# Kernel tuning notes

Measured on AMD Instinct MI355X. Metric: run time of the kernel, lower is better.

Reference implementation:

```python
import jax, jax.numpy as jnp
import numpy as np

N, E, G = 150000, 600000, 5000
NI, EI, GF, H, C = 16, 8, 32, 64, 40


def setup_inputs() -> dict:
    key = jax.random.key(0)
    ks = jax.random.split(key, 20)
    s = lambda fan: 1.0 / np.sqrt(fan)
    return {
        "x": jax.random.normal(ks[0], (N, NI), jnp.float32),
        "edge_index": jax.random.randint(ks[1], (2, E), 0, N),
        "edge_attr": jax.random.normal(ks[2], (E, EI), jnp.float32),
        "batch": jnp.sort(jax.random.randint(ks[3], (N,), 0, G)),
        "pocket_features": jax.random.normal(ks[4], (G, GF), jnp.float32),
        # edge MLP: Linear(EI,H) -> ReLU -> Linear(H, H*NI)
        "W_e1": jax.random.normal(ks[5], (EI, H), jnp.float32) * s(EI),
        "b_e1": jnp.zeros((H,), jnp.float32),
        "W_e2": jax.random.normal(ks[6], (H, H * NI), jnp.float32) * s(H),
        "b_e2": jnp.zeros((H * NI,), jnp.float32),
        # NNConv root weight + bias
        "root": jax.random.normal(ks[7], (NI, H), jnp.float32) * s(NI),
        "conv_bias": jnp.zeros((H,), jnp.float32),
        # GlobalAttention gate Linear(H,1)
        "Wg": jax.random.normal(ks[8], (H, 1), jnp.float32) * s(H),
        "bg": jnp.zeros((1,), jnp.float32),
        # fc1: input is concat [h_node(H), global_ctx(H), pocket(GF)]
        "W_fc1": jax.random.normal(ks[9], (2 * H + GF, H), jnp.float32) * s(2 * H + GF),
        "b_fc1": jnp.zeros((H,), jnp.float32),
        "W_np": jax.random.normal(ks[10], (H, C), jnp.float32) * s(H),
        "b_np": jnp.zeros((C,), jnp.float32),
        "W_sp": jax.random.normal(ks[11], (H, 1), jnp.float32) * s(H),
        "b_sp": jnp.zeros((1,), jnp.float32),
    }


def reference(x, edge_index, edge_attr, batch, pocket_features,
              W_e1, b_e1, W_e2, b_e2, root, conv_bias, Wg, bg,
              W_fc1, b_fc1, W_np, b_np, W_sp, b_sp):
    n, ni = x.shape
    h = root.shape[1]
    g = pocket_features.shape[0]
    src, dst = edge_index[0], edge_index[1]

    # NNConv: edge MLP -> per-edge weight matrix [E, NI, H]
    eh = jax.nn.relu(edge_attr @ W_e1 + b_e1)
    We = (eh @ W_e2 + b_e2).reshape(-1, ni, h)
    msg = jnp.einsum('ei,eih->eh', x[src], We)          # per-edge matmul
    agg = jax.ops.segment_sum(msg, dst, num_segments=n)
    cnt = jax.ops.segment_sum(jnp.ones(msg.shape[0], x.dtype), dst, num_segments=n)
    agg = agg / jnp.maximum(cnt, 1.0)[:, None]          # aggr='mean'
    h_node = jax.nn.relu(agg + x @ root + conv_bias)    # [N, H]

    # GlobalAttention pooling: scatter-softmax over nodes per graph
    gate = (h_node @ Wg + bg).squeeze(-1)               # [N]
    m = jax.ops.segment_max(gate, batch, num_segments=g)
    e = jnp.exp(gate - m[batch])
    denom = jax.ops.segment_sum(e, batch, num_segments=g)
    attn = e / denom[batch]
    gctx = jax.ops.segment_sum(attn[:, None] * h_node, batch, num_segments=g)
    gc = gctx[batch]                                    # broadcast back [N, H]

    feat = jnp.concatenate([h_node, gc, pocket_features[batch]], axis=1)
    f = jax.nn.relu(feat @ W_fc1 + b_fc1)
    node_pred = jax.nn.log_softmax(f @ W_np + b_np, axis=-1)
    stop = jax.nn.sigmoid((gc @ W_sp + b_sp).squeeze(-1))
    return node_pred, stop
```

## Files before the change

kernel.cpp:

```cpp
#include <hip/hip_runtime.h>
#include <hip/hip_bf16.h>
#include <math.h>

#define NN 150000
#define EE 600000
#define GG 5000
#define NI 16
#define EI 8
#define GFD 32
#define HH 64
#define CC 40

#define W2SZ (68 * 1024)
#define FPAD 68
#define NBLK ((NN + 1023) / 1024)

typedef __attribute__((ext_vector_type(8))) short short8v;
typedef __attribute__((ext_vector_type(16))) float f32x16;
typedef __attribute__((ext_vector_type(2))) float f32x2;

__device__ __forceinline__ unsigned short f2bf(float f) {
    __hip_bfloat16 h = __float2bfloat16(f);
    return __builtin_bit_cast(unsigned short, h);
}
__device__ __forceinline__ float bf2f(unsigned short u) {
    return __uint_as_float(((unsigned)u) << 16);
}
__device__ __forceinline__ unsigned cvtpk(float lo, float hi) {
    unsigned r;
    asm("v_cvt_pk_bf16_f32 %0, %1, %2" : "=v"(r) : "v"(lo), "v"(hi));
    return r;
}
__device__ __forceinline__ f32x2 pkmul(f32x2 a, f32x2 b) {
    f32x2 p;
    asm("v_pk_mul_f32 %0, %1, %2" : "=v"(p) : "v"(a), "v"(b));
    return p;
}
__device__ __forceinline__ short8v zfrag(float eh, const f32x2 (&xs2)[4]) {
    f32x2 ehp; ehp[0] = eh; ehp[1] = eh;
    union { short8v v; unsigned u[4]; } A;
    #pragma unroll
    for (int q = 0; q < 4; ++q) {
        f32x2 p = pkmul(ehp, xs2[q]);
        A.u[q] = cvtpk(p[0], p[1]);
    }
    return A.v;
}
__device__ __forceinline__ short8v xfrag(const f32x2 (&xs2)[4]) {
    union { short8v v; unsigned u[4]; } A;
    #pragma unroll
    for (int q = 0; q < 4; ++q)
        A.u[q] = cvtpk(xs2[q][0], xs2[q][1]);
    return A.v;
}

__global__ void k0_prep(const float* __restrict__ W_e2, const float* __restrict__ b_e2,
                        const float* __restrict__ W_fc1, const float* __restrict__ W_np,
                        unsigned short* __restrict__ W2c,
                        unsigned short* __restrict__ W1aT,
                        unsigned short* __restrict__ W_npT,
                        int* __restrict__ cursor)
{
    int idx = blockIdx.x * 256 + threadIdx.x;
    if (idx < W2SZ) {
        int c = idx >> 10, rem = idx & 1023;
        int r = rem >> 4, kk = rem & 15;
        float v = 0.f;
        if (c < 64)       v = W_e2[c * 1024 + kk * 64 + r];
        else if (c == 64) v = b_e2[kk * 64 + r];
        W2c[idx] = f2bf(v);
    } else if (idx < W2SZ + 4096) {
        int i = idx - W2SZ;
        int h = i >> 6, k = i & 63;
        W1aT[i] = f2bf(W_fc1[k * 64 + h]);
    } else if (idx < W2SZ + 8192) {
        int i = idx - W2SZ - 4096;
        int c = i >> 6, h = i & 63;
        W_npT[i] = f2bf(c < CC ? W_np[h * CC + c] : 0.f);
    } else if (idx < W2SZ + 8192 + NN) {
        cursor[idx - W2SZ - 8192] = 0;
    }
}

__global__ void kE_local(const int* __restrict__ ei, int* __restrict__ cursor,
                         int* __restrict__ rank)
{
    int e = blockIdx.x * 256 + threadIdx.x;
    if (e < EE) rank[e] = atomicAdd(&cursor[ei[EE + e]], 1);
}

__global__ void kB_scan1(const int* __restrict__ cnt, int* __restrict__ base,
                         int* __restrict__ bsum)
{
    __shared__ int sS[256];
    int b = blockIdx.x, t = threadIdx.x;
    int i0 = b * 1024 + t * 4;
    int v0 = (i0 + 0 < NN) ? cnt[i0 + 0] : 0;
    int v1 = (i0 + 1 < NN) ? cnt[i0 + 1] : 0;
    int v2 = (i0 + 2 < NN) ? cnt[i0 + 2] : 0;
    int v3 = (i0 + 3 < NN) ? cnt[i0 + 3] : 0;
    int tot = v0 + v1 + v2 + v3;
    sS[t] = tot;
    __syncthreads();
    int acc = tot;
    for (int off = 1; off < 256; off <<= 1) {
        int xv = (t >= off) ? sS[t - off] : 0;
        __syncthreads();
        acc += xv;
        sS[t] = acc;
        __syncthreads();
    }
    int run = acc - tot;
    if (i0 + 0 < NN) base[i0 + 0] = run; run += v0;
    if (i0 + 1 < NN) base[i0 + 1] = run; run += v1;
    if (i0 + 2 < NN) base[i0 + 2] = run; run += v2;
    if (i0 + 3 < NN) base[i0 + 3] = run;
    if (t == 255) bsum[b] = acc;
}

__global__ void kC_scan2(int* __restrict__ bsum)
{
    __shared__ int sS[256];
    int t = threadIdx.x;
    int v = (t < NBLK) ? bsum[t] : 0;
    sS[t] = v;
    __syncthreads();
    int acc = v;
    for (int off = 1; off < 256; off <<= 1) {
        int xv = (t >= off) ? sS[t - off] : 0;
        __syncthreads();
        acc += xv;
        sS[t] = acc;
        __syncthreads();
    }
    if (t < NBLK) bsum[t] = acc - v;
}

__global__ void kD_scan3(int* __restrict__ base, const int* __restrict__ bsum)
{
    int i = blockIdx.x * 256 + threadIdx.x;
    if (i < NN) base[i] = base[i] + bsum[i >> 10];
    if (i == 0) base[NN] = EE;
}

__device__ __forceinline__ void mfma_step(
    const unsigned short (&sEHT)[65][256], int c, int pf,
    const unsigned short* __restrict__ Bq0, const unsigned short* __restrict__ Bq1,
    int mb, int mr, const f32x2 (&xs0)[4], const f32x2 (&xs1)[4],
    short8v& curb0, short8v& curb1,
    f32x16& acc00, f32x16& acc01, f32x16& acc10, f32x16& acc11)
{
    short8v n0 = *(const short8v*)(Bq0 + pf * 1024);
    short8v n1 = *(const short8v*)(Bq1 + pf * 1024);
    int cc = (c & 31) << 1;
    float eh0 = bf2f(sEHT[c][(mb + mr) ^ cc]);
    float eh1 = bf2f(sEHT[c][(mb + 32 + mr) ^ cc]);
    short8v a0 = zfrag(eh0, xs0);
    short8v a1 = zfrag(eh1, xs1);
    __builtin_amdgcn_s_setprio(1);
    acc00 = __builtin_amdgcn_mfma_f32_32x32x16_bf16(a0, curb0, acc00, 0, 0, 0);
    acc01 = __builtin_amdgcn_mfma_f32_32x32x16_bf16(a0, curb1, acc01, 0, 0, 0);
    acc10 = __builtin_amdgcn_mfma_f32_32x32x16_bf16(a1, curb0, acc10, 0, 0, 0);
    acc11 = __builtin_amdgcn_mfma_f32_32x32x16_bf16(a1, curb1, acc11, 0, 0, 0);
    __builtin_amdgcn_s_setprio(0);
    curb0 = n0; curb1 = n1;
}

template<bool TWOPHASE>
__global__ __launch_bounds__(256, 4) void k1_mfma(
    const float* __restrict__ x, const int* __restrict__ ei,
    const float* __restrict__ ea,
    const float* __restrict__ W_e1, const float* __restrict__ b_e1,
    const unsigned short* __restrict__ W2c,
    const int* __restrict__ rank, const int* __restrict__ base,
    unsigned* __restrict__ msg16, float* __restrict__ agg)
{
    __shared__ unsigned short sEHT[65][256];
    __shared__ int sIdx[256];

    const int t = threadIdx.x;
    const long long eb = (long long)blockIdx.x * 256;

    {
        long long ge = eb + t;
        if (ge < EE) {
            int d = ei[EE + ge];
            sIdx[t] = TWOPHASE ? (base[d] + rank[ge]) : d;
        } else {
            sIdx[t] = -1;
        }
        sEHT[64][t] = (unsigned short)0x3F80;
    }
    {
        const int k = t & 63;
        const int w = t >> 6;
        float w1[8];
        float b1 = b_e1[k];
        #pragma unroll
        for (int j = 0; j < 8; ++j) w1[j] = W_e1[j * 64 + k];
        #pragma unroll 4
        for (int r = 0; r < 64; ++r) {
            int e = w * 64 + r;
            long long ge = eb + e;
            float v = 0.f;
            if (ge < EE) {
                const float4* eap = (const float4*)(ea + ge * EI);
                float4 u0 = eap[0], u1 = eap[1];
                v = b1;
                v = fmaf(u0.x, w1[0], v); v = fmaf(u0.y, w1[1], v);
                v = fmaf(u0.z, w1[2], v); v = fmaf(u0.w, w1[3], v);
                v = fmaf(u1.x, w1[4], v); v = fmaf(u1.y, w1[5], v);
                v = fmaf(u1.z, w1[6], v); v = fmaf(u1.w, w1[7], v);
                v = fmaxf(v, 0.f);
            }
            sEHT[k][e ^ ((k & 31) << 1)] = f2bf(v);
        }
    }

    const int lane = t & 63;
    const int w = t >> 6;
    const int mr = lane & 31;
    const int half = lane >> 5;
    const int mb = w * 64;

    f32x2 xs0[4], xs1[4];
    {
        long long e0 = eb + mb + mr;
        long long e1 = eb + mb + 32 + mr;
        if (e0 < EE) {
            int s0 = ei[e0];
            const float4* xp = (const float4*)(x + (size_t)s0 * NI + half * 8);
            float4 u0 = xp[0], u1 = xp[1];
            xs0[0][0]=u0.x; xs0[0][1]=u0.y; xs0[1][0]=u0.z; xs0[1][1]=u0.w;
            xs0[2][0]=u1.x; xs0[2][1]=u1.y; xs0[3][0]=u1.z; xs0[3][1]=u1.w;
        } else {
            #pragma unroll
            for (int q = 0; q < 4; ++q) { xs0[q][0] = 0.f; xs0[q][1] = 0.f; }
        }
        if (e1 < EE) {
            int s1 = ei[e1];
            const float4* xp = (const float4*)(x + (size_t)s1 * NI + half * 8);
            float4 u0 = xp[0], u1 = xp[1];
            xs1[0][0]=u0.x; xs1[0][1]=u0.y; xs1[1][0]=u0.z; xs1[1][1]=u0.w;
            xs1[2][0]=u1.x; xs1[2][1]=u1.y; xs1[3][0]=u1.z; xs1[3][1]=u1.w;
        } else {
            #pragma unroll
            for (int q = 0; q < 4; ++q) { xs1[q][0] = 0.f; xs1[q][1] = 0.f; }
        }
    }
    __syncthreads();

    f32x16 acc00, acc01, acc10, acc11;
    #pragma unroll
    for (int r = 0; r < 16; ++r) { acc00[r] = 0.f; acc01[r] = 0.f; acc10[r] = 0.f; acc11[r] = 0.f; }

    const unsigned short* Bq0 = W2c + mr * 16 + half * 8;
    const unsigned short* Bq1 = Bq0 + 512;

    short8v bA0 = *(const short8v*)(Bq0);
    short8v bA1 = *(const short8v*)(Bq1);
    short8v bB0 = *(const short8v*)(Bq0 + 1024);
    short8v bB1 = *(const short8v*)(Bq1 + 1024);

    #pragma unroll 2
    for (int c = 0; c < 64; c += 2) {
        mfma_step(sEHT, c,     c + 2, Bq0, Bq1, mb, mr, xs0, xs1, bA0, bA1, acc00, acc01, acc10, acc11);
        mfma_step(sEHT, c + 1, c + 3, Bq0, Bq1, mb, mr, xs0, xs1, bB0, bB1, acc00, acc01, acc10, acc11);
    }
    {
        short8v a0 = xfrag(xs0);
        short8v a1 = xfrag(xs1);
        __builtin_amdgcn_s_setprio(1);
        acc00 = __builtin_amdgcn_mfma_f32_32x32x16_bf16(a0, bA0, acc00, 0, 0, 0);
        acc01 = __builtin_amdgcn_mfma_f32_32x32x16_bf16(a0, bA1, acc01, 0, 0, 0);
        acc10 = __builtin_amdgcn_mfma_f32_32x32x16_bf16(a1, bA0, acc10, 0, 0, 0);
        acc11 = __builtin_amdgcn_mfma_f32_32x32x16_bf16(a1, bA1, acc11, 0, 0, 0);
        __builtin_amdgcn_s_setprio(0);
    }

    #pragma unroll
    for (int r = 0; r < 16; ++r) {
        int row = (r & 3) + 8 * (r >> 2) + 4 * half;
        int i0 = sIdx[mb + row];
        int i1 = sIdx[mb + 32 + row];
        if (TWOPHASE) {
            if (i0 >= 0) msg16[(size_t)i0 * 32 + mr] = cvtpk(acc00[r], acc01[r]);
            if (i1 >= 0) msg16[(size_t)i1 * 32 + mr] = cvtpk(acc10[r], acc11[r]);
        } else {
            if (i0 >= 0) {
                atomicAdd(&agg[(size_t)i0 * 64 + mr],      acc00[r]);
                atomicAdd(&agg[(size_t)i0 * 64 + 32 + mr], acc01[r]);
            }
            if (i1 >= 0) {
                atomicAdd(&agg[(size_t)i1 * 64 + mr],      acc10[r]);
                atomicAdd(&agg[(size_t)i1 * 64 + 32 + mr], acc11[r]);
            }
        }
    }
}

__global__ __launch_bounds__(256) void k2_red(
    const unsigned* __restrict__ msg16, const int* __restrict__ base,
    const float* __restrict__ x, const float* __restrict__ root,
    const float* __restrict__ conv_bias,
    unsigned short* __restrict__ hn16,
    const float* __restrict__ Wg, const float* __restrict__ bg,
    float* __restrict__ gate)
{
    __shared__ float sroot[16][64];
    int t = threadIdx.x;
    #pragma unroll
    for (int q = 0; q < 4; ++q) {
        int i = q * 256 + t;
        sroot[i >> 6][i & 63] = root[i];
    }
    __syncthreads();

    int n = blockIdx.x * 4 + (t >> 6);
    int l = t & 63;
    int mr = l & 31, so = l >> 5;
    int s = base[n], e = base[n + 1];

    float alo = 0.f, ahi = 0.f;
    for (int sl = s + so; sl < e; sl += 2) {
        unsigned u = msg16[(size_t)sl * 32 + mr];
        alo += __uint_as_float(u << 16);
        ahi += __uint_as_float(u & 0xFFFF0000u);
    }
    alo += __shfl_xor(alo, 32);
    ahi += __shfl_xor(ahi, 32);
    float acc = (l < 32) ? alo : ahi;

    float inv = 1.0f / fmaxf((float)(e - s), 1.0f);
    float v = acc * inv + conv_bias[l];
    float xv = (l < 16) ? x[(size_t)n * NI + l] : 0.f;
    #pragma unroll
    for (int i = 0; i < 16; ++i)
        v = fmaf(__shfl(xv, i), sroot[i][l], v);
    v = fmaxf(v, 0.f);
    hn16[(size_t)n * 64 + l] = f2bf(v);

    float gv = v * Wg[l];
    #pragma unroll
    for (int off = 32; off; off >>= 1) gv += __shfl_xor(gv, off);
    if (l == 0) gate[n] = gv + bg[0];
}

__global__ __launch_bounds__(256) void k2_node(
    const float* __restrict__ agg, const int* __restrict__ base,
    const float* __restrict__ x, const float* __restrict__ root,
    const float* __restrict__ conv_bias,
    unsigned short* __restrict__ hn16,
    const float* __restrict__ Wg, const float* __restrict__ bg,
    float* __restrict__ gate)
{
    int t = threadIdx.x;
    int n = blockIdx.x * 4 + (t >> 6);
    int h = t & 63;
    float cntv = (float)(base[n + 1] - base[n]);
    float inv = 1.0f / fmaxf(cntv, 1.0f);
    float v = agg[(size_t)n * 64 + h] * inv + conv_bias[h];
    const float* xp = x + (size_t)n * NI;
    #pragma unroll
    for (int i = 0; i < NI; ++i) v += xp[i] * root[i * 64 + h];
    v = fmaxf(v, 0.f);
    hn16[(size_t)n * 64 + h] = f2bf(v);
    float gv = v * Wg[h];
    #pragma unroll
    for (int off = 32; off; off >>= 1) gv += __shfl_xor(gv, off);
    if (h == 0) gate[n] = gv + bg[0];
}

__device__ __forceinline__ int lbound(const int* __restrict__ b, int v) {
    int lo = 0, hi = NN;
    while (lo < hi) { int mid = (lo + hi) >> 1; if (b[mid] < v) lo = mid + 1; else hi = mid; }
    return lo;
}

__global__ __launch_bounds__(64) void k3_pool(
    const float* __restrict__ gate, const int* __restrict__ batch,
    const unsigned short* __restrict__ hn16, const float* __restrict__ pocket,
    const float* __restrict__ W_fc1, const float* __restrict__ b_fc1,
    const float* __restrict__ W_sp, const float* __restrict__ b_sp,
    float* __restrict__ pg, float* __restrict__ sg)
{
    int g = blockIdx.x;
    int lane = threadIdx.x;
    int s = lbound(batch, g);
    int e = lbound(batch, g + 1);

    float gcv = 0.f;
    if (e > s) {
        float m = -INFINITY;
        for (int n = s + lane; n < e; n += 64) m = fmaxf(m, gate[n]);
        #pragma unroll
        for (int off = 32; off; off >>= 1) m = fmaxf(m, __shfl_xor(m, off));
        float acc = 0.f, den = 0.f;
        for (int n = s; n < e; ++n) {
            float ev = expf(gate[n] - m);
            den += ev;
            acc += ev * bf2f(hn16[(size_t)n * 64 + lane]);
        }
        gcv = acc / den;
    }

    float sv = gcv * W_sp[lane];
    #pragma unroll
    for (int off = 32; off; off >>= 1) sv += __shfl_xor(sv, off);
    if (lane == 0) sg[g] = 1.f / (1.f + expf(-(sv + b_sp[0])));

    float pk = (lane < GFD) ? pocket[(size_t)g * GFD + lane] : 0.f;
    float pgv = b_fc1[lane];
    #pragma unroll 8
    for (int kk = 0; kk < 64; ++kk)
        pgv = fmaf(__shfl(gcv, kk), W_fc1[(64 + kk) * 64 + lane], pgv);
    #pragma unroll 8
    for (int kk = 0; kk < 32; ++kk)
        pgv = fmaf(__shfl(pk, kk), W_fc1[(128 + kk) * 64 + lane], pgv);
    pg[(size_t)g * 64 + lane] = pgv;
}

__global__ __launch_bounds__(256, 4) void k4_mfma(
    const unsigned short* __restrict__ hn16, const int* __restrict__ batch,
    const float* __restrict__ pg, const float* __restrict__ sg,
    const unsigned short* __restrict__ W1aT, const unsigned short* __restrict__ W_npT,
    const float* __restrict__ b_np,
    float* __restrict__ out_np, float* __restrict__ out_stop)
{
    __shared__ __align__(16) float sF[4][32][FPAD];
    __shared__ int sB[128];

    const int t = threadIdx.x;
    const int wv = t >> 6, lane = t & 63;
    const int mr = lane & 31, half = lane >> 5;
    const int nb = blockIdx.x * 128;

    if (t < 128) {
        int n = nb + t;
        sB[t] = (n < NN) ? batch[n] : 0;
    }

    const int node = nb + wv * 32 + mr;

    f32x16 acc0, acc1;
    #pragma unroll
    for (int r = 0; r < 16; ++r) { acc0[r] = 0.f; acc1[r] = 0.f; }

    #pragma unroll
    for (int c = 0; c < 4; ++c) {
        short8v a;
        if (node < NN) {
            a = *(const short8v*)(hn16 + (size_t)node * 64 + c * 16 + half * 8);
        } else {
            #pragma unroll
            for (int q = 0; q < 8; ++q) a[q] = 0;
        }
        short8v b0 = *(const short8v*)(W1aT + (size_t)mr * 64        + c * 16 + half * 8);
        short8v b1 = *(const short8v*)(W1aT + (size_t)(mr + 32) * 64 + c * 16 + half * 8);
        acc0 = __builtin_amdgcn_mfma_f32_32x32x16_bf16(a, b0, acc0, 0, 0, 0);
        acc1 = __builtin_amdgcn_mfma_f32_32x32x16_bf16(a, b1, acc1, 0, 0, 0);
    }
    __syncthreads();

    #pragma unroll
    for (int r = 0; r < 16; ++r) {
        int row = (r & 3) + 8 * (r >> 2) + 4 * half;
        int g = sB[wv * 32 + row];
        float p0 = pg[(size_t)g * 64 + mr];
        float p1 = pg[(size_t)g * 64 + 32 + mr];
        sF[wv][row][mr]      = fmaxf(acc0[r] + p0, 0.f);
        sF[wv][row][32 + mr] = fmaxf(acc1[r] + p1, 0.f);
    }

    f32x16 acc2, acc3;
    #pragma unroll
    for (int r = 0; r < 16; ++r) { acc2[r] = 0.f; acc3[r] = 0.f; }

    #pragma unroll
    for (int c = 0; c < 4; ++c) {
        const float* fp = &sF[wv][mr][c * 16 + half * 8];
        float4 u0 = *(const float4*)(fp);
        float4 u1 = *(const float4*)(fp + 4);
        union { short8v v; unsigned u[4]; } A;
        A.u[0] = cvtpk(u0.x, u0.y); A.u[1] = cvtpk(u0.z, u0.w);
        A.u[2] = cvtpk(u1.x, u1.y); A.u[3] = cvtpk(u1.z, u1.w);
        short8v a = A.v;
        short8v b0 = *(const short8v*)(W_npT + (size_t)mr * 64        + c * 16 + half * 8);
        short8v b1 = *(const short8v*)(W_npT + (size_t)(mr + 32) * 64 + c * 16 + half * 8);
        acc2 = __builtin_amdgcn_mfma_f32_32x32x16_bf16(a, b0, acc2, 0, 0, 0);
        acc3 = __builtin_amdgcn_mfma_f32_32x32x16_bf16(a, b1, acc3, 0, 0, 0);
    }

    float bn1 = b_np[mr];
    float bn2 = (mr < 8) ? b_np[32 + mr] : 0.f;

    #pragma unroll
    for (int r = 0; r < 16; ++r) {
        int row = (r & 3) + 8 * (r >> 2) + 4 * half;
        int n = nb + wv * 32 + row;
        float v1 = acc2[r] + bn1;
        float v2 = acc3[r] + bn2;
        float m = (mr < 8) ? fmaxf(v1, v2) : v1;
        #pragma unroll
        for (int off = 16; off; off >>= 1) m = fmaxf(m, __shfl_xor(m, off));
        float s = expf(v1 - m) + ((mr < 8) ? expf(v2 - m) : 0.f);
        #pragma unroll
        for (int off = 16; off; off >>= 1) s += __shfl_xor(s, off);
        float ls = m + logf(s);
        if (n < NN) {
            out_np[(size_t)n * CC + mr] = v1 - ls;
            if (mr < 8) out_np[(size_t)n * CC + 32 + mr] = v2 - ls;
            if (mr == 0) out_stop[n] = sg[sB[wv * 32 + row]];
        }
    }
}

extern "C" void kernel_launch(void* const* d_in, const int* in_sizes, int n_in,
                              void* d_out, int out_size, void* d_ws, size_t ws_size,
                              hipStream_t stream)
{
    (void)in_sizes; (void)n_in; (void)out_size;
    const float* x        = (const float*)d_in[0];
    const int*   ei       = (const int*)d_in[1];
    const float* ea       = (const float*)d_in[2];
    const int*   batch    = (const int*)d_in[3];
    const float* pocket   = (const float*)d_in[4];
    const float* W_e1     = (const float*)d_in[5];
    const float* b_e1     = (const float*)d_in[6];
    const float* W_e2     = (const float*)d_in[7];
    const float* b_e2     = (const float*)d_in[8];
    const float* root     = (const float*)d_in[9];
    const float* conv_b   = (const float*)d_in[10];
    const float* Wg       = (const float*)d_in[11];
    const float* bg       = (const float*)d_in[12];
    const float* W_fc1    = (const float*)d_in[13];
    const float* b_fc1    = (const float*)d_in[14];
    const float* W_np     = (const float*)d_in[15];
    const float* b_np     = (const float*)d_in[16];
    const float* W_sp     = (const float*)d_in[17];
    const float* b_sp     = (const float*)d_in[18];

    char* wsb = (char*)d_ws;
    float* agg    = (float*)wsb;
    int*   base   = (int*)(agg + (size_t)NN * 64);
    int*   bsum   = base + NN + 4;
    int*   cursor = bsum + 256;
    int*   rank   = cursor + NN;
    float* gate   = (float*)(rank + EE);
    float* pg     = gate + NN;
    float* sg     = pg + (size_t)GG * 64;
    unsigned short* hn16  = (unsigned short*)(sg + GG);
    unsigned short* W2c   = hn16 + (size_t)NN * 64;
    unsigned short* W1aT  = W2c + W2SZ;
    unsigned short* W_npT = W1aT + 4096;
    size_t head = (size_t)((char*)(W_npT + 4096) - wsb);
    size_t msg_off = (head + 255) & ~(size_t)255;
    unsigned* msg16 = (unsigned*)(wsb + msg_off);
    size_t need = msg_off + (size_t)EE * 32 * sizeof(unsigned);
    const bool twophase = (ws_size >= need);

    k0_prep<<<(W2SZ + 8192 + NN + 255) / 256, 256, 0, stream>>>(
        W_e2, b_e2, W_fc1, W_np, W2c, W1aT, W_npT, cursor);

    kE_local<<<(EE + 255) / 256, 256, 0, stream>>>(ei, cursor, rank);
    kB_scan1<<<NBLK, 256, 0, stream>>>(cursor, base, bsum);
    kC_scan2<<<1, 256, 0, stream>>>(bsum);
    kD_scan3<<<(NN + 255) / 256, 256, 0, stream>>>(base, bsum);

    if (twophase) {
        k1_mfma<true><<<(EE + 255) / 256, 256, 0, stream>>>(
            x, ei, ea, W_e1, b_e1, W2c, rank, base, msg16, agg);
        k2_red<<<NN / 4, 256, 0, stream>>>(msg16, base, x, root, conv_b,
                                           hn16, Wg, bg, gate);
    } else {
        hipMemsetAsync(agg, 0, (size_t)NN * 64 * sizeof(float), stream);
        k1_mfma<false><<<(EE + 255) / 256, 256, 0, stream>>>(
            x, ei, ea, W_e1, b_e1, W2c, rank, base, msg16, agg);
        k2_node<<<NN / 4, 256, 0, stream>>>(agg, base, x, root, conv_b, hn16, Wg, bg, gate);
    }

    k3_pool<<<GG, 64, 0, stream>>>(gate, batch, hn16, pocket, W_fc1, b_fc1, W_sp, b_sp, pg, sg);

    float* out_np   = (float*)d_out;
    float* out_stop = out_np + (size_t)NN * CC;
    k4_mfma<<<(NN + 127) / 128, 256, 0, stream>>>(hn16, batch, pg, sg, W1aT, W_npT, b_np,
                                                  out_np, out_stop);
}
```

Before: 297.5 us.

## Compute edge MLP first layer with MFMA and fold scan fixup into consumers

```diff
diff --git a/kernel.cpp b/kernel.cpp
--- a/kernel.cpp
+++ b/kernel.cpp
@@ -56,9 +56,11 @@
 
 __global__ void k0_prep(const float* __restrict__ W_e2, const float* __restrict__ b_e2,
                         const float* __restrict__ W_fc1, const float* __restrict__ W_np,
+                        const float* __restrict__ W_e1,
                         unsigned short* __restrict__ W2c,
                         unsigned short* __restrict__ W1aT,
                         unsigned short* __restrict__ W_npT,
+                        unsigned short* __restrict__ W1e,
                         int* __restrict__ cursor)
 {
     int idx = blockIdx.x * 256 + threadIdx.x;
@@ -77,8 +79,12 @@
         int i = idx - W2SZ - 4096;
         int c = i >> 6, h = i & 63;
         W_npT[i] = f2bf(c < CC ? W_np[h * CC + c] : 0.f);
-    } else if (idx < W2SZ + 8192 + NN) {
-        cursor[idx - W2SZ - 8192] = 0;
+    } else if (idx < W2SZ + 8704) {
+        int i = idx - W2SZ - 8192;
+        int col = i >> 3, q = i & 7;
+        W1e[i] = f2bf(W_e1[q * 64 + col]);
+    } else if (idx < W2SZ + 8704 + NN) {
+        cursor[idx - W2SZ - 8704] = 0;
     }
 }
 
@@ -136,13 +142,6 @@
     if (t < NBLK) bsum[t] = acc - v;
 }
 
-__global__ void kD_scan3(int* __restrict__ base, const int* __restrict__ bsum)
-{
-    int i = blockIdx.x * 256 + threadIdx.x;
-    if (i < NN) base[i] = base[i] + bsum[i >> 10];
-    if (i == 0) base[NN] = EE;
-}
-
 __device__ __forceinline__ void mfma_step(
     const unsigned short (&sEHT)[65][256], int c, int pf,
     const unsigned short* __restrict__ Bq0, const unsigned short* __restrict__ Bq1,
@@ -170,9 +169,10 @@
 __global__ __launch_bounds__(256, 4) void k1_mfma(
     const float* __restrict__ x, const int* __restrict__ ei,
     const float* __restrict__ ea,
-    const float* __restrict__ W_e1, const float* __restrict__ b_e1,
+    const unsigned short* __restrict__ W1e, const float* __restrict__ b_e1,
     const unsigned short* __restrict__ W2c,
     const int* __restrict__ rank, const int* __restrict__ base,
+    const int* __restrict__ bsum,
     unsigned* __restrict__ msg16, float* __restrict__ agg)
 {
     __shared__ unsigned short sEHT[65][256];
@@ -180,48 +180,70 @@
 
     const int t = threadIdx.x;
     const long long eb = (long long)blockIdx.x * 256;
-
-    {
-        long long ge = eb + t;
-        if (ge < EE) {
-            int d = ei[EE + ge];
-            sIdx[t] = TWOPHASE ? (base[d] + rank[ge]) : d;
-        } else {
-            sIdx[t] = -1;
-        }
-        sEHT[64][t] = (unsigned short)0x3F80;
-    }
-    {
-        const int k = t & 63;
-        const int w = t >> 6;
-        float w1[8];
-        float b1 = b_e1[k];
-        #pragma unroll
-        for (int j = 0; j < 8; ++j) w1[j] = W_e1[j * 64 + k];
-        #pragma unroll 4
-        for (int r = 0; r < 64; ++r) {
-            int e = w * 64 + r;
-            long long ge = eb + e;
-            float v = 0.f;
-            if (ge < EE) {
-                const float4* eap = (const float4*)(ea + ge * EI);
-                float4 u0 = eap[0], u1 = eap[1];
-                v = b1;
-                v = fmaf(u0.x, w1[0], v); v = fmaf(u0.y, w1[1], v);
-                v = fmaf(u0.z, w1[2], v); v = fmaf(u0.w, w1[3], v);
-                v = fmaf(u1.x, w1[4], v); v = fmaf(u1.y, w1[5], v);
-                v = fmaf(u1.z, w1[6], v); v = fmaf(u1.w, w1[7], v);
-                v = fmaxf(v, 0.f);
-            }
-            sEHT[k][e ^ ((k & 31) << 1)] = f2bf(v);
-        }
-    }
 
     const int lane = t & 63;
     const int w = t >> 6;
     const int mr = lane & 31;
     const int half = lane >> 5;
     const int mb = w * 64;
+
+    {
+        long long ge = eb + t;
+        if (ge < EE) {
+            int d = ei[EE + ge];
+            sIdx[t] = TWOPHASE ? (base[d] + bsum[d >> 10] + rank[ge]) : d;
+        } else {
+            sIdx[t] = -1;
+        }
+        sEHT[64][t] = (unsigned short)0x3F80;
+    }
+
+    {
+        short8v bW0, bW1;
+        if (half == 0) {
+            bW0 = *(const short8v*)(W1e + (size_t)mr * 8);
+            bW1 = *(const short8v*)(W1e + (size_t)(32 + mr) * 8);
+        } else {
+            #pragma unroll
+            for (int q = 0; q < 8; ++q) { bW0[q] = 0; bW1[q] = 0; }
+        }
+        float bias0 = b_e1[mr];
+        float bias1 = b_e1[32 + mr];
+        #pragma unroll
+        for (int m = 0; m < 2; ++m) {
+            int e_loc = w * 64 + m * 32 + mr;
+            long long ge = eb + e_loc;
+            short8v a;
+            if (half == 0 && ge < EE) {
+                const float4* eap = (const float4*)(ea + ge * EI);
+                float4 u0 = eap[0], u1 = eap[1];
+                union { short8v v; unsigned u[4]; } A;
+                A.u[0] = cvtpk(u0.x, u0.y); A.u[1] = cvtpk(u0.z, u0.w);
+                A.u[2] = cvtpk(u1.x, u1.y); A.u[3] = cvtpk(u1.z, u1.w);
+                a = A.v;
+            } else {
+                #pragma unroll
+                for (int q = 0; q < 8; ++q) a[q] = 0;
+            }
+            #pragma unroll
+            for (int n = 0; n < 2; ++n) {
+                f32x16 c_;
+                #pragma unroll
+                for (int r = 0; r < 16; ++r) c_[r] = 0.f;
+                c_ = __builtin_amdgcn_mfma_f32_32x32x16_bf16(a, n ? bW1 : bW0, c_, 0, 0, 0);
+                int kcol = n * 32 + mr;
+                float bias = n ? bias1 : bias0;
+                #pragma unroll
+                for (int r = 0; r < 16; r += 2) {
+                    int row = (r & 3) + 8 * (r >> 2) + 4 * half;
+                    int e0 = w * 64 + m * 32 + row;
+                    float v0 = fmaxf(c_[r]     + bias, 0.f);
+                    float v1 = fmaxf(c_[r + 1] + bias, 0.f);
+                    *(unsigned*)&sEHT[kcol][e0 ^ (mr << 1)] = cvtpk(v0, v1);
+                }
+            }
+        }
+    }
 
     f32x2 xs0[4], xs1[4];
     {
@@ -301,6 +323,7 @@
 
 __global__ __launch_bounds__(256) void k2_red(
     const unsigned* __restrict__ msg16, const int* __restrict__ base,
+    const int* __restrict__ bsum,
     const float* __restrict__ x, const float* __restrict__ root,
     const float* __restrict__ conv_bias,
     unsigned short* __restrict__ hn16,
@@ -319,7 +342,8 @@
     int n = blockIdx.x * 4 + (t >> 6);
     int l = t & 63;
     int mr = l & 31, so = l >> 5;
-    int s = base[n], e = base[n + 1];
+    int s = base[n] + bsum[n >> 10];
+    int e = (n == NN - 1) ? EE : base[n + 1] + bsum[(n + 1) >> 10];
 
     float alo = 0.f, ahi = 0.f;
     for (int sl = s + so; sl < e; sl += 2) {
@@ -348,6 +372,7 @@
 
 __global__ __launch_bounds__(256) void k2_node(
     const float* __restrict__ agg, const int* __restrict__ base,
+    const int* __restrict__ bsum,
     const float* __restrict__ x, const float* __restrict__ root,
     const float* __restrict__ conv_bias,
     unsigned short* __restrict__ hn16,
@@ -357,8 +382,9 @@
     int t = threadIdx.x;
     int n = blockIdx.x * 4 + (t >> 6);
     int h = t & 63;
-    float cntv = (float)(base[n + 1] - base[n]);
-    float inv = 1.0f / fmaxf(cntv, 1.0f);
+    int s = base[n] + bsum[n >> 10];
+    int e = (n == NN - 1) ? EE : base[n + 1] + bsum[(n + 1) >> 10];
+    float inv = 1.0f / fmaxf((float)(e - s), 1.0f);
     float v = agg[(size_t)n * 64 + h] * inv + conv_bias[h];
     const float* xp = x + (size_t)n * NI;
     #pragma unroll
@@ -553,30 +579,31 @@
     unsigned short* W2c   = hn16 + (size_t)NN * 64;
     unsigned short* W1aT  = W2c + W2SZ;
     unsigned short* W_npT = W1aT + 4096;
-    size_t head = (size_t)((char*)(W_npT + 4096) - wsb);
+    unsigned short* W1e   = W_npT + 4096;
+    size_t head = (size_t)((char*)(W1e + 512) - wsb);
     size_t msg_off = (head + 255) & ~(size_t)255;
     unsigned* msg16 = (unsigned*)(wsb + msg_off);
     size_t need = msg_off + (size_t)EE * 32 * sizeof(unsigned);
     const bool twophase = (ws_size >= need);
 
-    k0_prep<<<(W2SZ + 8192 + NN + 255) / 256, 256, 0, stream>>>(
-        W_e2, b_e2, W_fc1, W_np, W2c, W1aT, W_npT, cursor);
+    k0_prep<<<(W2SZ + 8704 + NN + 255) / 256, 256, 0, stream>>>(
+        W_e2, b_e2, W_fc1, W_np, W_e1, W2c, W1aT, W_npT, W1e, cursor);
 
     kE_local<<<(EE + 255) / 256, 256, 0, stream>>>(ei, cursor, rank);
     kB_scan1<<<NBLK, 256, 0, stream>>>(cursor, base, bsum);
     kC_scan2<<<1, 256, 0, stream>>>(bsum);
-    kD_scan3<<<(NN + 255) / 256, 256, 0, stream>>>(base, bsum);
 
     if (twophase) {
         k1_mfma<true><<<(EE + 255) / 256, 256, 0, stream>>>(
-            x, ei, ea, W_e1, b_e1, W2c, rank, base, msg16, agg);
-        k2_red<<<NN / 4, 256, 0, stream>>>(msg16, base, x, root, conv_b,
+            x, ei, ea, W1e, b_e1, W2c, rank, base, bsum, msg16, agg);
+        k2_red<<<NN / 4, 256, 0, stream>>>(msg16, base, bsum, x, root, conv_b,
                                            hn16, Wg, bg, gate);
     } else {
         hipMemsetAsync(agg, 0, (size_t)NN * 64 * sizeof(float), stream);
         k1_mfma<false><<<(EE + 255) / 256, 256, 0, stream>>>(
-            x, ei, ea, W_e1, b_e1, W2c, rank, base, msg16, agg);
-        k2_node<<<NN / 4, 256, 0, stream>>>(agg, base, x, root, conv_b, hn16, Wg, bg, gate);
+            x, ei, ea, W1e, b_e1, W2c, rank, base, bsum, msg16, agg);
+        k2_node<<<NN / 4, 256, 0, stream>>>(agg, base, bsum, x, root, conv_b,
+                                            hn16, Wg, bg, gate);
     }
 
     k3_pool<<<GG, 64, 0, stream>>>(gate, batch, hn16, pocket, W_fc1, b_fc1, W_sp, b_sp, pg, sg);
```

After: 259.9 us. 1.14x faster.
